# Kernel optimization log

Measured on AMD Instinct MI355X. Metric: run time of the kernel, lower is better.

The kernel has to match this reference:

```python
import jax, jax.numpy as jnp
import numpy as np

SEQ_LEN, BATCH, INPUT, HID, LAYERS, TARGET_LEN = 120, 2048, 6, 64, 4, 120


def _cell(x_t, h, c, Wih, Whh, b):
    # torch LSTM gate order: input, forget, cell(g), output
    gates = x_t @ Wih.T + h @ Whh.T + b  # [B, 4H]
    i, f, g, o = jnp.split(gates, 4, axis=-1)
    c_new = jax.nn.sigmoid(f) * c + jax.nn.sigmoid(i) * jnp.tanh(g)
    h_new = jax.nn.sigmoid(o) * jnp.tanh(c_new)
    return h_new, c_new


def _stack_step(h, c, x_t, Wih0, Wih, Whh, b):
    # one time step through all stacked layers; h, c: [L, B, H]
    hs, cs = [], []
    inp = x_t
    L = Whh.shape[0]
    for l in range(L):
        W = Wih0 if l == 0 else Wih[l - 1]
        hn, cn = _cell(inp, h[l], c[l], W, Whh[l], b[l])
        hs.append(hn)
        cs.append(cn)
        inp = hn
    return jnp.stack(hs), jnp.stack(cs), inp


def setup_inputs() -> dict:
    key = jax.random.key(0)
    ks = jax.random.split(key, 11)
    s = 1.0 / np.sqrt(HID)  # torch LSTM uniform init scale
    u = lambda k, shp: jax.random.uniform(k, shp, jnp.float32, -s, s)
    return {
        "x": jax.random.normal(ks[0], (SEQ_LEN, BATCH, INPUT), jnp.float32),
        "enc_Wih0": u(ks[1], (4 * HID, INPUT)),
        "enc_Wih": u(ks[2], (LAYERS - 1, 4 * HID, HID)),
        "enc_Whh": u(ks[3], (LAYERS, 4 * HID, HID)),
        "enc_b": u(ks[4], (LAYERS, 4 * HID)),
        "dec_Wih0": u(ks[5], (4 * HID, INPUT)),
        "dec_Wih": u(ks[6], (LAYERS - 1, 4 * HID, HID)),
        "dec_Whh": u(ks[7], (LAYERS, 4 * HID, HID)),
        "dec_b": u(ks[8], (LAYERS, 4 * HID)),
        "lin_W": u(ks[9], (INPUT, HID)),
        "lin_b": u(ks[10], (INPUT,)),
        "target_len": TARGET_LEN,
    }


def reference(x, enc_Wih0, enc_Wih, enc_Whh, enc_b,
              dec_Wih0, dec_Wih, dec_Whh, dec_b, lin_W, lin_b, target_len):
    L, B, H = enc_Whh.shape[0], x.shape[1], enc_Whh.shape[-1]
    h0 = jnp.zeros((L, B, H), x.dtype)

    # ---- encoder: stacked LSTM over the input sequence (zero init state) ----
    def enc_step(carry, x_t):
        h, c = carry
        h, c, _ = _stack_step(h, c, x_t, enc_Wih0, enc_Wih, enc_Whh, enc_b)
        return (h, c), None

    (h, c), _ = jax.lax.scan(enc_step, (h0, h0), x)

    # ---- decoder: recursive one-step decode for target_len steps ----
    def dec_step(carry, _):
        h, c, inp = carry
        h, c, top = _stack_step(h, c, inp, dec_Wih0, dec_Wih, dec_Whh, dec_b)
        out = top @ lin_W.T + lin_b  # [B, INPUT]
        return (h, c, out), out

    last_in = x[-1]  # decoder seeded with last observed frame
    _, outputs = jax.lax.scan(dec_step, (h, c, last_in), None, length=target_len)
    return outputs  # [target_len, B, INPUT]
```

## Files before the change

### kernel.cpp

```cpp
#include <hip/hip_runtime.h>


#define S_LEN 120
#define BATCH 2048
#define NIN   6
#define H     64
#define NL    4
#define TLEN  120

#define HPAD 72

#define FRAGS_HALF 60
#define PACK_H8    (2 * FRAGS_HALF * 4 * 64)
#define PROJ_H8    (2 * 64)
#define NPACK      ((PACK_H8 + PROJ_H8) * 8)
#define EPACK_EL   (256 * 64 * 8)
#define NTOT       (NPACK + EPACK_EL)

#define PERM(kk) ((((kk) & 3) << 4) | ((kk) >> 2))
#define PI(c)    ((((c) & 15) << 2) | ((c) >> 4))

typedef _Float16 h8    __attribute__((ext_vector_type(8)));
typedef _Float16 h4    __attribute__((ext_vector_type(4)));
typedef float    f32x4 __attribute__((ext_vector_type(4)));

__global__ void prep_weights(const float* __restrict__ eWih0,
                             const float* __restrict__ eWih,
                             const float* __restrict__ eWhh,
                             const float* __restrict__ dWih0,
                             const float* __restrict__ dWih,
                             const float* __restrict__ dWhh,
                             const float* __restrict__ linW,
                             _Float16* __restrict__ wq) {
  int idx = blockIdx.x * blockDim.x + threadIdx.x;
  if (idx >= NTOT) return;

  if (idx >= NPACK) {
    int p    = idx - NPACK;
    int j    = p & 7;
    int lane = (p >> 3) & 63;
    int fe   = p >> 9;
    int kt   = fe & 3, nt = (fe >> 2) & 15, l = fe >> 6;
    int g    = nt * 16 + (lane & 15);
    int koff = ((lane >> 4) << 3) + j;
    float v = 0.0f;
    if (l == 0) {
      if (kt == 0)      v = (koff < NIN) ? eWih0[g * NIN + koff] : 0.0f;
      else if (kt == 1) v = 0.0f;
      else { int kk = (kt - 2) * 32 + koff; v = eWhh[g * H + PERM(kk)]; }
    } else {
      if (kt < 2) { int kk = kt * 32 + koff;
                    v = eWih[((l - 1) * 256 + g) * H + PERM(kk)]; }
      else        { int kk = (kt - 2) * 32 + koff;
                    v = eWhh[(l * 256 + g) * H + PERM(kk)]; }
    }
    wq[idx] = (_Float16)v;
    return;
  }

  if (idx >= PACK_H8 * 8) {
    int p    = idx - PACK_H8 * 8;
    int j    = p & 7;
    int lane = (p >> 3) & 63;
    int fr   = p >> 9;
    int m    = lane & 15;
    int k    = fr * 32 + ((lane >> 4) << 3) + j;
    wq[idx] = (_Float16)((m < NIN) ? linW[m * H + k] : 0.0f);
    return;
  }

  const int j    = idx & 7;
  const int lane = (idx >> 3) & 63;
  const int wv   = (idx >> 9) & 3;
  const int fh   = idx >> 11;
  const int f    = fh % FRAGS_HALF;
  const int half = fh / FRAGS_HALF;
  const float* Wi0 = half ? dWih0 : eWih0;
  const float* Wi  = half ? dWih  : eWih;
  const float* Wh  = half ? dWhh  : eWhh;
  int l, q, kt;
  if (f < 12) { l = 0; q = f / 3; kt = f % 3; }
  else        { int ff = f - 12; l = 1 + ff / 16; ff %= 16; q = ff / 4; kt = ff % 4; }
  const int g    = q * 64 + wv * 16 + (lane & 15);
  const int k_in = ((lane >> 4) << 3) + j;
  float v;
  if (l == 0) {
    if (kt == 0) v = (k_in < NIN) ? Wi0[g * NIN + k_in] : 0.0f;
    else         v = Wh[g * H + (kt - 1) * 32 + k_in];
  } else {
    if (kt < 2) v = Wi[((l - 1) * 256 + g) * H + kt * 32 + k_in];
    else        v = Wh[(l * 256 + g) * H + (kt - 2) * 32 + k_in];
  }
  wq[idx] = (_Float16)v;
}

__device__ __forceinline__ float rcpf(float x) { return __builtin_amdgcn_rcpf(x); }
__device__ __forceinline__ float sigf(float x) { return rcpf(1.0f + __expf(-x)); }
__device__ __forceinline__ float tanhf_(float x) {
  float e = __expf(2.0f * x);
  return 1.0f - 2.0f * rcpf(e + 1.0f);
}
__device__ __forceinline__ f32x4 mf(h8 a, h8 b, f32x4 c) {
  return __builtin_amdgcn_mfma_f32_16x16x32_f16(a, b, c, 0, 0, 0);
}
#define SPLAT(v) ((f32x4){(v), (v), (v), (v)})

__device__ __forceinline__ void cell_ew(f32x4 g0, f32x4 g1, f32x4 g2, f32x4 g3,
                                        f32x4& c, _Float16* outbuf,
                                        int quad, int r16, int wv) {
  #pragma unroll
  for (int r = 0; r < 4; r++) {
    float gi = sigf(g0[r]);
    float gf = sigf(g1[r]);
    float gg = tanhf_(g2[r]);
    float go = sigf(g3[r]);
    c[r] = fmaf(gf, c[r], gi * gg);
    outbuf[(quad * 4 + r) * HPAD + wv * 16 + r16] = (_Float16)(go * tanhf_(c[r]));
  }
}
__device__ __forceinline__ void fireH(const h8 (&w)[16], h8 ai0, h8 ai1,
                                      const f32x4 (&ac)[4], f32x4& c,
                                      _Float16* outbuf, int quad, int r16, int wv) {
  f32x4 g0 = mf(ai1, w[1],  mf(ai0, w[0],  ac[0]));
  f32x4 g1 = mf(ai1, w[5],  mf(ai0, w[4],  ac[1]));
  f32x4 g2 = mf(ai1, w[9],  mf(ai0, w[8],  ac[2]));
  f32x4 g3 = mf(ai1, w[13], mf(ai0, w[12], ac[3]));
  cell_ew(g0, g1, g2, g3, c, outbuf, quad, r16, wv);
}
__device__ __forceinline__ void precH(const h8 (&w)[16], h8 ar0, h8 ar1,
                                      f32x4 b, f32x4 (&ac)[4]) {
  ac[0] = mf(ar1, w[3],  mf(ar0, w[2],  SPLAT(b[0])));
  ac[1] = mf(ar1, w[7],  mf(ar0, w[6],  SPLAT(b[1])));
  ac[2] = mf(ar1, w[11], mf(ar0, w[10], SPLAT(b[2])));
  ac[3] = mf(ar1, w[15], mf(ar0, w[14], SPLAT(b[3])));
}
__device__ __forceinline__ void fire0(const h8 (&w)[12], h8 ax,
                                      const f32x4 (&ac)[4], f32x4& c,
                                      _Float16* outbuf, int quad, int r16, int wv) {
  f32x4 g0 = mf(ax, w[0], ac[0]);
  f32x4 g1 = mf(ax, w[3], ac[1]);
  f32x4 g2 = mf(ax, w[6], ac[2]);
  f32x4 g3 = mf(ax, w[9], ac[3]);
  cell_ew(g0, g1, g2, g3, c, outbuf, quad, r16, wv);
}
__device__ __forceinline__ void prec0(const h8 (&w)[12], h8 ar0, h8 ar1,
                                      f32x4 b, f32x4 (&ac)[4]) {
  ac[0] = mf(ar1, w[2],  mf(ar0, w[1],  SPLAT(b[0])));
  ac[1] = mf(ar1, w[5],  mf(ar0, w[4],  SPLAT(b[1])));
  ac[2] = mf(ar1, w[8],  mf(ar0, w[7],  SPLAT(b[2])));
  ac[3] = mf(ar1, w[11], mf(ar0, w[10], SPLAT(b[3])));
}
__device__ __forceinline__ void readA(const _Float16* buf, int r16, int quad,
                                      h8& a0, h8& a1) {
  a0 = *(const h8*)(buf + r16 * HPAD + quad * 8);
  a1 = *(const h8*)(buf + r16 * HPAD + 32 + quad * 8);
}

__global__ void __launch_bounds__(256, 1)
lstm_main(const float* __restrict__ X,
          const float* __restrict__ encb,
          const float* __restrict__ decb,
          const float* __restrict__ linb,
          const h8* __restrict__ WQ,
          float* __restrict__ out) {
  __shared__ _Float16 Hb[NL][2][16][HPAD];
  __shared__ _Float16 Xb[2][16][HPAD];
  __shared__ float    Cx[NL][16][68];

  const int tid   = threadIdx.x;
  const int wv    = tid >> 6;
  const int lane  = tid & 63;
  const int quad  = lane >> 4;
  const int r16   = lane & 15;
  const int bbase = blockIdx.x * 16;

  {
    float* p = (float*)&Hb[0][0][0][0];
    for (int i = tid; i < (int)(NL * 2 * 16 * HPAD / 2); i += 256) p[i] = 0.0f;
    float* px = (float*)&Xb[0][0][0];
    for (int i = tid; i < (int)(2 * 16 * HPAD / 2); i += 256) px[i] = 0.0f;
  }
  if (tid < 96) {
    const int m = tid / NIN, i = tid - m * NIN;
    Xb[0][m][i] = (_Float16)X[((size_t)0 * BATCH + bbase + m) * NIN + i];
  }

  h8 we[16][4];
  #pragma unroll
  for (int nt = 0; nt < 16; nt++)
    #pragma unroll
    for (int kt = 0; kt < 4; kt++)
      we[nt][kt] = WQ[(PACK_H8 + PROJ_H8) + ((wv * 64 + nt * 4 + kt) * 64 + lane)];

  float ben[16];
  #pragma unroll
  for (int nt = 0; nt < 16; nt++) ben[nt] = encb[wv * 256 + nt * 16 + r16];

  f32x4 ce[4];
  #pragma unroll
  for (int ct = 0; ct < 4; ct++) ce[ct] = SPLAT(0.f);

  __syncthreads();

  #pragma unroll 1
  for (int i = 0; i < S_LEN + NL - 1; i++) {
    const int p = i & 1;
    const bool active = (i >= wv) && (i - wv < S_LEN);
    if (active) {
      const _Float16* inb = (wv == 0) ? &Xb[p][0][0] : &Hb[wv - 1][p ^ 1][0][0];
      const _Float16* rcb = &Hb[wv][p ^ 1][0][0];
      h8 ai0 = *(const h8*)(inb + r16 * HPAD + quad * 8);
      h8 ai1 = *(const h8*)(inb + r16 * HPAD + 32 + quad * 8);
      h8 ar0 = *(const h8*)(rcb + r16 * HPAD + quad * 8);
      h8 ar1 = *(const h8*)(rcb + r16 * HPAD + 32 + quad * 8);

      float pf0 = 0.f, pf1 = 0.f;
      const bool doPf = (wv == 0) && (lane < 48) && (i + 1 < S_LEN);
      if (doPf) {
        const float* xs = X + ((size_t)(i + 1) * BATCH + bbase) * NIN;
        pf0 = xs[lane * 2];
        pf1 = xs[lane * 2 + 1];
      }

      f32x4 acc[16];
      #pragma unroll
      for (int nt = 0; nt < 16; nt++) {
        f32x4 a = SPLAT(ben[nt]);
        a = mf(ai0, we[nt][0], a);
        a = mf(ai1, we[nt][1], a);
        a = mf(ar0, we[nt][2], a);
        a = mf(ar1, we[nt][3], a);
        acc[nt] = a;
      }

      _Float16* wb = &Hb[wv][p][0][0];
      #pragma unroll
      for (int r = 0; r < 4; r++) {
        h4 hv;
        #pragma unroll
        for (int ct = 0; ct < 4; ct++) {
          float gi = sigf(acc[ct][r]);
          float gf = sigf(acc[4 + ct][r]);
          float gg = tanhf_(acc[8 + ct][r]);
          float go = sigf(acc[12 + ct][r]);
          ce[ct][r] = fmaf(gf, ce[ct][r], gi * gg);
          hv[ct] = (_Float16)(go * tanhf_(ce[ct][r]));
        }
        *(h4*)(wb + (quad * 4 + r) * HPAD + 4 * r16) = hv;
      }

      if (doPf) {
        int e0 = lane * 2, e1 = e0 + 1;
        Xb[p ^ 1][e0 / NIN][e0 % NIN] = (_Float16)pf0;
        Xb[p ^ 1][e1 / NIN][e1 % NIN] = (_Float16)pf1;
      }
    }
    __syncthreads();
  }

  #pragma unroll
  for (int ct = 0; ct < 4; ct++)
    #pragma unroll
    for (int r = 0; r < 4; r++)
      Cx[wv][quad * 4 + r][ct * 16 + r16] = ce[ct][r];

  float hreg[16];
  #pragma unroll
  for (int u = 0; u < 16; u++) {
    int i2 = tid + u * 256;
    int l = i2 >> 10, m = (i2 >> 6) & 15, c = i2 & 63;
    hreg[u] = (float)Hb[l][(l + 1) & 1][m][PI(c)];
  }
  __syncthreads();
  #pragma unroll
  for (int u = 0; u < 16; u++) {
    int i2 = tid + u * 256;
    int l = i2 >> 10, m = (i2 >> 6) & 15, c = i2 & 63;
    Hb[l][1][m][c] = (_Float16)hreg[u];
  }
  __syncthreads();

  f32x4 cs0, cs1, cs2, cs3;
  #pragma unroll
  for (int r = 0; r < 4; r++) {
    cs0[r] = Cx[0][quad * 4 + r][wv * 16 + r16];
    cs1[r] = Cx[1][quad * 4 + r][wv * 16 + r16];
    cs2[r] = Cx[2][quad * 4 + r][wv * 16 + r16];
    cs3[r] = Cx[3][quad * 4 + r][wv * 16 + r16];
  }

  h8 w0[12], w1[16], w2[16], w3[16];
  #pragma unroll
  for (int f = 0; f < 12; f++) w0[f] = WQ[((FRAGS_HALF + f)      * 4 + wv) * 64 + lane];
  #pragma unroll
  for (int f = 0; f < 16; f++) w1[f] = WQ[((FRAGS_HALF + 12 + f) * 4 + wv) * 64 + lane];
  #pragma unroll
  for (int f = 0; f < 16; f++) w2[f] = WQ[((FRAGS_HALF + 28 + f) * 4 + wv) * 64 + lane];
  #pragma unroll
  for (int f = 0; f < 16; f++) w3[f] = WQ[((FRAGS_HALF + 44 + f) * 4 + wv) * 64 + lane];

  f32x4 b0, b1, b2, b3;
  #pragma unroll
  for (int q = 0; q < 4; q++) {
    b0[q] = decb[0 * 256 + q * 64 + wv * 16 + r16];
    b1[q] = decb[1 * 256 + q * 64 + wv * 16 + r16];
    b2[q] = decb[2 * 256 + q * 64 + wv * 16 + r16];
    b3[q] = decb[3 * 256 + q * 64 + wv * 16 + r16];
  }

  h8 lwA0 = WQ[PACK_H8 + lane];
  h8 lwA1 = WQ[PACK_H8 + 64 + lane];
  f32x4 lbq;
  #pragma unroll
  for (int r = 0; r < 4; r++)
    lbq[r] = (quad * 4 + r < NIN) ? linb[quad * 4 + r] : 0.0f;

  f32x4 ac0[4], ac1[4], ac2[4], ac3[4];
  {
    h8 s0, s1;
    readA(&Hb[0][1][0][0], r16, quad, s0, s1); prec0(w0, s0, s1, b0, ac0);
    readA(&Hb[1][1][0][0], r16, quad, s0, s1); precH(w1, s0, s1, b1, ac1);
    readA(&Hb[2][1][0][0], r16, quad, s0, s1); precH(w2, s0, s1, b2, ac2);
  }
  __syncthreads();

  #pragma unroll 1
  for (int t = 0; t < TLEN; t++) {
    const int cur = t & 1, prv = cur ^ 1;
    {
      h8 ar0, ar1;
      readA(&Hb[3][prv][0][0], r16, quad, ar0, ar1);
      h8 ax;
      if (t == 0) {
        ax = *(const h8*)(&Xb[1][0][0] + r16 * HPAD + quad * 8);
      } else {
        f32x4 ap = lbq;
        ap = mf(lwA0, ar0, ap);
        ap = mf(lwA1, ar1, ap);
        if (wv == 0) {
          #pragma unroll
          for (int r = 0; r < 4; r++) {
            const int fm = quad * 4 + r;
            if (fm < NIN)
              out[((size_t)(t - 1) * BATCH + bbase + r16) * NIN + fm] = ap[r];
          }
        }
        float x0 = __shfl(ap[0], r16);
        float x1 = __shfl(ap[1], r16);
        float x2 = __shfl(ap[2], r16);
        float x3 = __shfl(ap[3], r16);
        float x4 = __shfl(ap[0], 16 + r16);
        float x5 = __shfl(ap[1], 16 + r16);
        h8 xa = {};
        xa[0] = (_Float16)x0; xa[1] = (_Float16)x1; xa[2] = (_Float16)x2;
        xa[3] = (_Float16)x3; xa[4] = (_Float16)x4; xa[5] = (_Float16)x5;
        h8 zz = {};
        ax = (quad == 0) ? xa : zz;
      }
      precH(w3, ar0, ar1, b3, ac3);
      fire0(w0, ax, ac0, cs0, &Hb[0][cur][0][0], quad, r16, wv);
      __syncthreads();
    }
    {
      h8 ai0, ai1;
      readA(&Hb[0][cur][0][0], r16, quad, ai0, ai1);
      fireH(w1, ai0, ai1, ac1, cs1, &Hb[1][cur][0][0], quad, r16, wv);
      prec0(w0, ai0, ai1, b0, ac0);
      __syncthreads();
    }
    {
      h8 ai0, ai1;
      readA(&Hb[1][cur][0][0], r16, quad, ai0, ai1);
      fireH(w2, ai0, ai1, ac2, cs2, &Hb[2][cur][0][0], quad, r16, wv);
      precH(w1, ai0, ai1, b1, ac1);
      __syncthreads();
    }
    {
      h8 ai0, ai1;
      readA(&Hb[2][cur][0][0], r16, quad, ai0, ai1);
      fireH(w3, ai0, ai1, ac3, cs3, &Hb[3][cur][0][0], quad, r16, wv);
      precH(w2, ai0, ai1, b2, ac2);
      __syncthreads();
    }
  }

  if (wv == 0) {
    h8 ar0, ar1;
    readA(&Hb[3][1][0][0], r16, quad, ar0, ar1);
    f32x4 ap = lbq;
    ap = mf(lwA0, ar0, ap);
    ap = mf(lwA1, ar1, ap);
    #pragma unroll
    for (int r = 0; r < 4; r++) {
      const int fm = quad * 4 + r;
      if (fm < NIN)
        out[((size_t)(TLEN - 1) * BATCH + bbase + r16) * NIN + fm] = ap[r];
    }
  }
}

extern "C" void kernel_launch(void* const* d_in, const int* in_sizes, int n_in,
                              void* d_out, int out_size, void* d_ws, size_t ws_size,
                              hipStream_t stream) {
  const float* X     = (const float*)d_in[0];
  const float* eWih0 = (const float*)d_in[1];
  const float* eWih  = (const float*)d_in[2];
  const float* eWhh  = (const float*)d_in[3];
  const float* eb    = (const float*)d_in[4];
  const float* dWih0 = (const float*)d_in[5];
  const float* dWih  = (const float*)d_in[6];
  const float* dWhh  = (const float*)d_in[7];
  const float* db    = (const float*)d_in[8];
  const float* lW    = (const float*)d_in[9];
  const float* lb    = (const float*)d_in[10];

  _Float16* wq = (_Float16*)d_ws;

  prep_weights<<<(NTOT + 255) / 256, 256, 0, stream>>>(
      eWih0, eWih, eWhh, dWih0, dWih, dWhh, lW, wq);

  lstm_main<<<BATCH / 16, 256, 0, stream>>>(
      X, eb, db, lb, (const h8*)wq, (float*)d_out);
}
```

Baseline: 579.4 us.

## Halve batch rows per block and split gate activations across lane halves

Each block now handles 8 batch rows instead of 16, doubling the grid to 256 blocks so more of the GPU's compute units are busy. The MFMA tiles still span 16 rows, half of them padding. Lanes swap accumulator halves via cross-lane shuffles, so each lane evaluates the gate nonlinearities for 2 rows instead of 4, shortening the serial elementwise tail. The activation maths is also fused to use fewer reciprocals. The cost is wasted MFMA work on padded rows, extra shuffles, and weights reloaded by twice as many blocks.

Measured after the change: 618.4 us. 1.07x slower.

```diff
diff --git a/kernel.cpp b/kernel.cpp
--- a/kernel.cpp
+++ b/kernel.cpp
@@ -7,6 +7,7 @@
 #define H     64
 #define NL    4
 #define TLEN  120
+#define BB    8
 
 #define HPAD 72
 
@@ -95,37 +96,50 @@
 }
 
 __device__ __forceinline__ float rcpf(float x) { return __builtin_amdgcn_rcpf(x); }
-__device__ __forceinline__ float sigf(float x) { return rcpf(1.0f + __expf(-x)); }
-__device__ __forceinline__ float tanhf_(float x) {
-  float e = __expf(2.0f * x);
-  return 1.0f - 2.0f * rcpf(e + 1.0f);
-}
 __device__ __forceinline__ f32x4 mf(h8 a, h8 b, f32x4 c) {
   return __builtin_amdgcn_mfma_f32_16x16x32_f16(a, b, c, 0, 0, 0);
 }
 #define SPLAT(v) ((f32x4){(v), (v), (v), (v)})
 
-__device__ __forceinline__ void cell_ew(f32x4 g0, f32x4 g1, f32x4 g2, f32x4 g3,
-                                        f32x4& c, _Float16* outbuf,
-                                        int quad, int r16, int wv) {
-  #pragma unroll
-  for (int r = 0; r < 4; r++) {
-    float gi = sigf(g0[r]);
-    float gf = sigf(g1[r]);
-    float gg = tanhf_(g2[r]);
-    float go = sigf(g3[r]);
-    c[r] = fmaf(gf, c[r], gi * gg);
-    outbuf[(quad * 4 + r) * HPAD + wv * 16 + r16] = (_Float16)(go * tanhf_(c[r]));
-  }
-}
+__device__ __forceinline__ float ew_one(float gi, float gf, float gg, float go,
+                                        float& c) {
+  gg = fminf(fmaxf(gg, -20.0f), 20.0f);
+  float eni = __expf(-gi);
+  float e2g = __expf(2.0f * gg);
+  float enf = __expf(-gf);
+  float eno = __expf(-go);
+  c = c * rcpf(1.0f + enf) + (e2g - 1.0f) * rcpf((1.0f + eni) * (e2g + 1.0f));
+  float cc = fminf(fmaxf(c, -20.0f), 20.0f);
+  float e2c = __expf(2.0f * cc);
+  return (e2c - 1.0f) * rcpf((1.0f + eno) * (e2c + 1.0f));
+}
+
+__device__ __forceinline__ void ew_store2(f32x4 g0, f32x4 g1, f32x4 g2, f32x4 g3,
+                                          float2& c2, _Float16* outbuf,
+                                          int rowA, bool hi, int colOff) {
+  float pi0 = __shfl_xor(g0[2], 32), pi1 = __shfl_xor(g0[3], 32);
+  float pf0 = __shfl_xor(g1[2], 32), pf1 = __shfl_xor(g1[3], 32);
+  float pg0 = __shfl_xor(g2[2], 32), pg1 = __shfl_xor(g2[3], 32);
+  float po0 = __shfl_xor(g3[2], 32), po1 = __shfl_xor(g3[3], 32);
+  float i0 = hi ? pi0 : g0[0], i1 = hi ? pi1 : g0[1];
+  float f0 = hi ? pf0 : g1[0], f1 = hi ? pf1 : g1[1];
+  float q0 = hi ? pg0 : g2[0], q1 = hi ? pg1 : g2[1];
+  float o0 = hi ? po0 : g3[0], o1 = hi ? po1 : g3[1];
+  float h0v = ew_one(i0, f0, q0, o0, c2.x);
+  float h1v = ew_one(i1, f1, q1, o1, c2.y);
+  outbuf[rowA * HPAD + colOff]       = (_Float16)h0v;
+  outbuf[(rowA + 1) * HPAD + colOff] = (_Float16)h1v;
+}
+
 __device__ __forceinline__ void fireH(const h8 (&w)[16], h8 ai0, h8 ai1,
-                                      const f32x4 (&ac)[4], f32x4& c,
-                                      _Float16* outbuf, int quad, int r16, int wv) {
+                                      const f32x4 (&ac)[4], float2& c2,
+                                      _Float16* outbuf, int rowA, bool hi,
+                                      int colOff) {
   f32x4 g0 = mf(ai1, w[1],  mf(ai0, w[0],  ac[0]));
   f32x4 g1 = mf(ai1, w[5],  mf(ai0, w[4],  ac[1]));
   f32x4 g2 = mf(ai1, w[9],  mf(ai0, w[8],  ac[2]));
   f32x4 g3 = mf(ai1, w[13], mf(ai0, w[12], ac[3]));
-  cell_ew(g0, g1, g2, g3, c, outbuf, quad, r16, wv);
+  ew_store2(g0, g1, g2, g3, c2, outbuf, rowA, hi, colOff);
 }
 __device__ __forceinline__ void precH(const h8 (&w)[16], h8 ar0, h8 ar1,
                                       f32x4 b, f32x4 (&ac)[4]) {
@@ -135,13 +149,14 @@
   ac[3] = mf(ar1, w[15], mf(ar0, w[14], SPLAT(b[3])));
 }
 __device__ __forceinline__ void fire0(const h8 (&w)[12], h8 ax,
-                                      const f32x4 (&ac)[4], f32x4& c,
-                                      _Float16* outbuf, int quad, int r16, int wv) {
+                                      const f32x4 (&ac)[4], float2& c2,
+                                      _Float16* outbuf, int rowA, bool hi,
+                                      int colOff) {
   f32x4 g0 = mf(ax, w[0], ac[0]);
   f32x4 g1 = mf(ax, w[3], ac[1]);
   f32x4 g2 = mf(ax, w[6], ac[2]);
   f32x4 g3 = mf(ax, w[9], ac[3]);
-  cell_ew(g0, g1, g2, g3, c, outbuf, quad, r16, wv);
+  ew_store2(g0, g1, g2, g3, c2, outbuf, rowA, hi, colOff);
 }
 __device__ __forceinline__ void prec0(const h8 (&w)[12], h8 ar0, h8 ar1,
                                       f32x4 b, f32x4 (&ac)[4]) {
@@ -165,14 +180,16 @@
           float* __restrict__ out) {
   __shared__ _Float16 Hb[NL][2][16][HPAD];
   __shared__ _Float16 Xb[2][16][HPAD];
-  __shared__ float    Cx[NL][16][68];
+  __shared__ float    Cx[NL][BB][68];
 
   const int tid   = threadIdx.x;
   const int wv    = tid >> 6;
   const int lane  = tid & 63;
   const int quad  = lane >> 4;
   const int r16   = lane & 15;
-  const int bbase = blockIdx.x * 16;
+  const bool hi   = quad >= 2;
+  const int rowA  = hi ? (quad - 2) * 4 + 2 : quad * 4;
+  const int bbase = blockIdx.x * BB;
 
   {
     float* p = (float*)&Hb[0][0][0][0];
@@ -180,9 +197,9 @@
     float* px = (float*)&Xb[0][0][0];
     for (int i = tid; i < (int)(2 * 16 * HPAD / 2); i += 256) px[i] = 0.0f;
   }
-  if (tid < 96) {
-    const int m = tid / NIN, i = tid - m * NIN;
-    Xb[0][m][i] = (_Float16)X[((size_t)0 * BATCH + bbase + m) * NIN + i];
+  if (tid < BB * NIN) {
+    const int m = tid / NIN, ii = tid - m * NIN;
+    Xb[0][m][ii] = (_Float16)X[((size_t)0 * BATCH + bbase + m) * NIN + ii];
   }
 
   h8 we[16][4];
@@ -196,9 +213,9 @@
   #pragma unroll
   for (int nt = 0; nt < 16; nt++) ben[nt] = encb[wv * 256 + nt * 16 + r16];
 
-  f32x4 ce[4];
-  #pragma unroll
-  for (int ct = 0; ct < 4; ct++) ce[ct] = SPLAT(0.f);
+  float2 ce2[4];
+  #pragma unroll
+  for (int ct = 0; ct < 4; ct++) ce2[ct] = make_float2(0.f, 0.f);
 
   __syncthreads();
 
@@ -214,12 +231,11 @@
       h8 ar0 = *(const h8*)(rcb + r16 * HPAD + quad * 8);
       h8 ar1 = *(const h8*)(rcb + r16 * HPAD + 32 + quad * 8);
 
-      float pf0 = 0.f, pf1 = 0.f;
-      const bool doPf = (wv == 0) && (lane < 48) && (i + 1 < S_LEN);
+      float pfv = 0.f; int pm = 0, pix = 0;
+      const bool doPf = (wv == 0) && (lane < BB * NIN) && (i + 1 < S_LEN);
       if (doPf) {
-        const float* xs = X + ((size_t)(i + 1) * BATCH + bbase) * NIN;
-        pf0 = xs[lane * 2];
-        pf1 = xs[lane * 2 + 1];
+        pm = lane / NIN; pix = lane - pm * NIN;
+        pfv = X[((size_t)(i + 1) * BATCH + bbase + pm) * NIN + pix];
       }
 
       f32x4 acc[16];
@@ -233,61 +249,60 @@
         acc[nt] = a;
       }
 
+      float va[16][2];
+      #pragma unroll
+      for (int nt = 0; nt < 16; nt++) {
+        float a2 = __shfl_xor(acc[nt][2], 32);
+        float a3 = __shfl_xor(acc[nt][3], 32);
+        va[nt][0] = hi ? a2 : acc[nt][0];
+        va[nt][1] = hi ? a3 : acc[nt][1];
+      }
+
       _Float16* wb = &Hb[wv][p][0][0];
       #pragma unroll
-      for (int r = 0; r < 4; r++) {
+      for (int s = 0; s < 2; s++) {
         h4 hv;
         #pragma unroll
         for (int ct = 0; ct < 4; ct++) {
-          float gi = sigf(acc[ct][r]);
-          float gf = sigf(acc[4 + ct][r]);
-          float gg = tanhf_(acc[8 + ct][r]);
-          float go = sigf(acc[12 + ct][r]);
-          ce[ct][r] = fmaf(gf, ce[ct][r], gi * gg);
-          hv[ct] = (_Float16)(go * tanhf_(ce[ct][r]));
+          float& cref = s ? ce2[ct].y : ce2[ct].x;
+          hv[ct] = (_Float16)ew_one(va[ct][s], va[4 + ct][s],
+                                    va[8 + ct][s], va[12 + ct][s], cref);
         }
-        *(h4*)(wb + (quad * 4 + r) * HPAD + 4 * r16) = hv;
-      }
-
-      if (doPf) {
-        int e0 = lane * 2, e1 = e0 + 1;
-        Xb[p ^ 1][e0 / NIN][e0 % NIN] = (_Float16)pf0;
-        Xb[p ^ 1][e1 / NIN][e1 % NIN] = (_Float16)pf1;
-      }
+        *(h4*)(wb + (rowA + s) * HPAD + 4 * r16) = hv;
+      }
+
+      if (doPf) Xb[p ^ 1][pm][pix] = (_Float16)pfv;
     }
     __syncthreads();
   }
 
   #pragma unroll
-  for (int ct = 0; ct < 4; ct++)
-    #pragma unroll
-    for (int r = 0; r < 4; r++)
-      Cx[wv][quad * 4 + r][ct * 16 + r16] = ce[ct][r];
-
-  float hreg[16];
-  #pragma unroll
-  for (int u = 0; u < 16; u++) {
+  for (int ct = 0; ct < 4; ct++) {
+    Cx[wv][rowA][ct * 16 + r16]     = ce2[ct].x;
+    Cx[wv][rowA + 1][ct * 16 + r16] = ce2[ct].y;
+  }
+
+  float hreg[8];
+  #pragma unroll
+  for (int u = 0; u < 8; u++) {
     int i2 = tid + u * 256;
-    int l = i2 >> 10, m = (i2 >> 6) & 15, c = i2 & 63;
+    int l = i2 >> 9, m = (i2 >> 6) & 7, c = i2 & 63;
     hreg[u] = (float)Hb[l][(l + 1) & 1][m][PI(c)];
   }
   __syncthreads();
   #pragma unroll
-  for (int u = 0; u < 16; u++) {
+  for (int u = 0; u < 8; u++) {
     int i2 = tid + u * 256;
-    int l = i2 >> 10, m = (i2 >> 6) & 15, c = i2 & 63;
+    int l = i2 >> 9, m = (i2 >> 6) & 7, c = i2 & 63;
     Hb[l][1][m][c] = (_Float16)hreg[u];
   }
   __syncthreads();
 
-  f32x4 cs0, cs1, cs2, cs3;
-  #pragma unroll
-  for (int r = 0; r < 4; r++) {
-    cs0[r] = Cx[0][quad * 4 + r][wv * 16 + r16];
-    cs1[r] = Cx[1][quad * 4 + r][wv * 16 + r16];
-    cs2[r] = Cx[2][quad * 4 + r][wv * 16 + r16];
-    cs3[r] = Cx[3][quad * 4 + r][wv * 16 + r16];
-  }
+  const int cw = wv * 16 + r16;
+  float2 cs0 = make_float2(Cx[0][rowA][cw], Cx[0][rowA + 1][cw]);
+  float2 cs1 = make_float2(Cx[1][rowA][cw], Cx[1][rowA + 1][cw]);
+  float2 cs2 = make_float2(Cx[2][rowA][cw], Cx[2][rowA + 1][cw]);
+  float2 cs3 = make_float2(Cx[3][rowA][cw], Cx[3][rowA + 1][cw]);
 
   h8 w0[12], w1[16], w2[16], w3[16];
   #pragma unroll
@@ -337,7 +352,7 @@
         f32x4 ap = lbq;
         ap = mf(lwA0, ar0, ap);
         ap = mf(lwA1, ar1, ap);
-        if (wv == 0) {
+        if (wv == 0 && r16 < BB) {
           #pragma unroll
           for (int r = 0; r < 4; r++) {
             const int fm = quad * 4 + r;
@@ -358,27 +373,27 @@
         ax = (quad == 0) ? xa : zz;
       }
       precH(w3, ar0, ar1, b3, ac3);
-      fire0(w0, ax, ac0, cs0, &Hb[0][cur][0][0], quad, r16, wv);
+      fire0(w0, ax, ac0, cs0, &Hb[0][cur][0][0], rowA, hi, cw);
       __syncthreads();
     }
     {
       h8 ai0, ai1;
       readA(&Hb[0][cur][0][0], r16, quad, ai0, ai1);
-      fireH(w1, ai0, ai1, ac1, cs1, &Hb[1][cur][0][0], quad, r16, wv);
+      fireH(w1, ai0, ai1, ac1, cs1, &Hb[1][cur][0][0], rowA, hi, cw);
       prec0(w0, ai0, ai1, b0, ac0);
       __syncthreads();
     }
     {
       h8 ai0, ai1;
       readA(&Hb[1][cur][0][0], r16, quad, ai0, ai1);
-      fireH(w2, ai0, ai1, ac2, cs2, &Hb[2][cur][0][0], quad, r16, wv);
+      fireH(w2, ai0, ai1, ac2, cs2, &Hb[2][cur][0][0], rowA, hi, cw);
       precH(w1, ai0, ai1, b1, ac1);
       __syncthreads();
     }
     {
       h8 ai0, ai1;
       readA(&Hb[2][cur][0][0], r16, quad, ai0, ai1);
-      fireH(w3, ai0, ai1, ac3, cs3, &Hb[3][cur][0][0], quad, r16, wv);
+      fireH(w3, ai0, ai1, ac3, cs3, &Hb[3][cur][0][0], rowA, hi, cw);
       precH(w2, ai0, ai1, b2, ac2);
       __syncthreads();
     }
@@ -390,11 +405,13 @@
     f32x4 ap = lbq;
     ap = mf(lwA0, ar0, ap);
     ap = mf(lwA1, ar1, ap);
-    #pragma unroll
-    for (int r = 0; r < 4; r++) {
-      const int fm = quad * 4 + r;
-      if (fm < NIN)
-        out[((size_t)(TLEN - 1) * BATCH + bbase + r16) * NIN + fm] = ap[r];
+    if (r16 < BB) {
+      #pragma unroll
+      for (int r = 0; r < 4; r++) {
+        const int fm = quad * 4 + r;
+        if (fm < NIN)
+          out[((size_t)(TLEN - 1) * BATCH + bbase + r16) * NIN + fm] = ap[r];
+      }
     }
   }
 }
@@ -419,6 +436,6 @@
   prep_weights<<<(NTOT + 255) / 256, 256, 0, stream>>>(
       eWih0, eWih, eWhh, dWih0, dWih, dWhh, lW, wq);
 
-  lstm_main<<<BATCH / 16, 256, 0, stream>>>(
+  lstm_main<<<BATCH / BB, 256, 0, stream>>>(
       X, eb, db, lb, (const h8*)wq, (float*)d_out);
 }
```
